# Optimization experiments

Measured on AMD Instinct MI355X. Metric: run time of the kernel, lower is better.

## Reference

```python
import jax, jax.numpy as jnp
import numpy as np

DIM = 1024
HEADS = 16
DIM_HEAD = 64
INNER = HEADS * DIM_HEAD
SCALE = DIM_HEAD ** -0.5
CAUSAL = True


def setup_inputs() -> dict:
    key = jax.random.key(0)
    k1, k2, k3, k4 = jax.random.split(key, 4)
    b, n = 4, 2048
    x = jax.random.normal(k1, (b, n, DIM), dtype=jnp.float32)
    mask = jnp.ones((b, n), dtype=bool)
    w_qkv = jax.random.normal(k2, (DIM, 3 * INNER), dtype=jnp.float32) * (DIM ** -0.5)
    w_out = jax.random.normal(k3, (INNER, DIM), dtype=jnp.float32) * (INNER ** -0.5)
    ln_g = jnp.ones((DIM,), dtype=jnp.float32)
    return {"x": x, "mask": mask, "w_qkv": w_qkv, "w_out": w_out, "ln_g": ln_g}


def clip_layernorm(x, g):
    eps = 1e-5 if x.dtype == jnp.float32 else 1e-3
    mean = jnp.mean(x, axis=-1, keepdims=True)
    var = jnp.var(x, axis=-1, keepdims=True)  # unbiased=False
    return (x - mean) * jax.lax.rsqrt(var + eps) * g


def reference(x, mask, w_qkv, w_out, ln_g):
    b, n, _ = x.shape
    qkv = x @ w_qkv  # [b, n, 3*inner]
    q, k, v = jnp.split(qkv, 3, axis=-1)
    split_heads = lambda t: t.reshape(b, n, HEADS, DIM_HEAD).transpose(0, 2, 1, 3)
    q, k, v = split_heads(q), split_heads(k), split_heads(v)
    q = q * SCALE
    sim = jnp.einsum('bhid,bhjd->bhij', q, k)
    mask_value = -jnp.finfo(sim.dtype).max
    sim = jnp.where(mask[:, None, None, :], sim, mask_value)
    if CAUSAL:
        causal_mask = jnp.triu(jnp.ones((n, n), dtype=bool), k=1)
        sim = jnp.where(causal_mask, mask_value, sim)
    attn = jax.nn.softmax(sim.astype(jnp.float32), axis=-1).astype(sim.dtype)
    out = jnp.einsum('bhij,bhjd->bhid', attn, v)
    out = out.transpose(0, 2, 1, 3).reshape(b, n, INNER)
    out = out @ w_out
    return clip_layernorm(out, ln_g)
```

## Files before the change

kernel.cpp:

```cpp
#include <hip/hip_runtime.h>


typedef unsigned short u16;
typedef __attribute__((ext_vector_type(8))) short bf16x8;
typedef __attribute__((ext_vector_type(4))) float f32x4;
typedef __attribute__((ext_vector_type(4))) unsigned short u16x4;
typedef __attribute__((ext_vector_type(2))) unsigned u32x2;

#define B_SZ  4
#define NSEQ  2048
#define DIMM  1024
#define NQKV  3072
#define MROWS 8192

#define AS_GLOBAL __attribute__((address_space(1)))
#define AS_LDS    __attribute__((address_space(3)))

__device__ __forceinline__ void async_copy16(void* lds, const void* g) {
  __builtin_amdgcn_global_load_lds((const AS_GLOBAL void*)g, (AS_LDS void*)lds, 16, 0, 0);
}

__device__ __forceinline__ u16 f32_to_bf16(float f) {
  unsigned u = __float_as_uint(f);
  u += 0x7FFFu + ((u >> 16) & 1u);
  return (u16)(u >> 16);
}

__device__ __forceinline__ unsigned cvt_pk_bf16(float a, float b) {
  unsigned r;
  asm("v_cvt_pk_bf16_f32 %0, %1, %2" : "=v"(r) : "v"(a), "v"(b));
  return r;
}


__global__ __launch_bounds__(256) void cvt_bf16_k(const float* __restrict__ in,
                                                  u16* __restrict__ out, int n4) {
  int i = blockIdx.x * 256 + threadIdx.x;
  if (i >= n4) return;
  f32x4 v = ((const f32x4*)in)[i];
  u16x4 o;
  #pragma unroll
  for (int c = 0; c < 4; ++c) o[c] = f32_to_bf16(v[c]);
  ((u16x4*)out)[i] = o;
}

__global__ __launch_bounds__(256) void tconv_k(const float* __restrict__ in,
                                               u16* __restrict__ out, int K, int N) {
  __shared__ float tile[64][65];
  int n0 = blockIdx.x * 64, k0 = blockIdx.y * 64;
  int t = threadIdx.x, tr = t >> 6, tc = t & 63;
  #pragma unroll
  for (int i = 0; i < 16; ++i)
    tile[tr + i * 4][tc] = in[(size_t)(k0 + tr + i * 4) * N + n0 + tc];
  __syncthreads();
  #pragma unroll
  for (int i = 0; i < 16; ++i)
    out[(size_t)(n0 + tr + i * 4) * K + k0 + tc] = f32_to_bf16(tile[tc][tr + i * 4]);
}


__device__ __forceinline__ void gemm_tile(const u16* __restrict__ A, const u16* __restrict__ Bt,
                                          int K, size_t arow0, size_t brow0,
                                          u16* lA, u16* lB, int t, f32x4 acc[4][4]) {
  const int w = t >> 6, l = t & 63;
  const int wr = (w >> 1) * 64, wc = (w & 1) * 64;
  const int l4 = l >> 4, l15 = l & 15;
  for (int kt = 0; kt < K; kt += 32) {
    __syncthreads();
    #pragma unroll
    for (int p = 0; p < 2; ++p) {
      int c = p * 256 + t;
      int row = c >> 2, c16 = c & 3;
      async_copy16(&lA[c * 8], &A[(arow0 + row) * (size_t)K + kt + c16 * 8]);
      async_copy16(&lB[c * 8], &Bt[(brow0 + row) * (size_t)K + kt + c16 * 8]);
    }
    __syncthreads();
    bf16x8 af[4], bfr[4];
    #pragma unroll
    for (int i = 0; i < 4; ++i) af[i] = *(const bf16x8*)&lA[(wr + i * 16 + l15) * 32 + l4 * 8];
    #pragma unroll
    for (int j = 0; j < 4; ++j) bfr[j] = *(const bf16x8*)&lB[(wc + j * 16 + l15) * 32 + l4 * 8];
    #pragma unroll
    for (int i = 0; i < 4; ++i)
      #pragma unroll
      for (int j = 0; j < 4; ++j)
        acc[i][j] = __builtin_amdgcn_mfma_f32_16x16x32_bf16(af[i], bfr[j], acc[i][j], 0, 0, 0);
  }
}

__global__ __launch_bounds__(256) void gemm_qkv_k(const u16* __restrict__ A, const u16* __restrict__ Bt,
                                                  u16* __restrict__ qb, u16* __restrict__ kb,
                                                  u16* __restrict__ vtb) {
  __shared__ u16 lA[4096], lB[4096];
  f32x4 acc[4][4];
  #pragma unroll
  for (int i = 0; i < 4; ++i)
    #pragma unroll
    for (int j = 0; j < 4; ++j) acc[i][j] = (f32x4){0.f, 0.f, 0.f, 0.f};
  const int t = threadIdx.x;
  gemm_tile(A, Bt, DIMM, (size_t)blockIdx.y * 128, (size_t)blockIdx.x * 128, lA, lB, t, acc);
  const int w = t >> 6, l = t & 63;
  const int wr = (w >> 1) * 64, wc = (w & 1) * 64;
  const int l4 = l >> 4, l15 = l & 15;
  const float QSCALE = 0.125f * 1.44269504089f;
  #pragma unroll
  for (int i = 0; i < 4; ++i)
    #pragma unroll
    for (int j = 0; j < 4; ++j)
      #pragma unroll
      for (int r = 0; r < 4; ++r) {
        int row = blockIdx.y * 128 + wr + i * 16 + l4 * 4 + r;
        int col = blockIdx.x * 128 + wc + j * 16 + l15;
        float v = acc[i][j][r];
        int bb = row >> 11, nr = row & 2047;
        int part = col >> 10, rem = col & 1023;
        int h = rem >> 6, d = rem & 63;
        int bh = bb * 16 + h;
        if (part == 0)      qb[((size_t)bh * NSEQ + nr) * 64 + d] = f32_to_bf16(v * QSCALE);
        else if (part == 1) kb[((size_t)bh * NSEQ + nr) * 64 + d] = f32_to_bf16(v);
        else                vtb[((size_t)bh * 64 + d) * NSEQ + nr] = f32_to_bf16(v);
      }
}

__global__ __launch_bounds__(256) void gemm_out_k(const u16* __restrict__ A, const u16* __restrict__ Bt,
                                                  float* __restrict__ C) {
  __shared__ u16 lA[4096], lB[4096];
  f32x4 acc[4][4];
  #pragma unroll
  for (int i = 0; i < 4; ++i)
    #pragma unroll
    for (int j = 0; j < 4; ++j) acc[i][j] = (f32x4){0.f, 0.f, 0.f, 0.f};
  const int t = threadIdx.x;
  gemm_tile(A, Bt, DIMM, (size_t)blockIdx.y * 128, (size_t)blockIdx.x * 128, lA, lB, t, acc);
  const int w = t >> 6, l = t & 63;
  const int wr = (w >> 1) * 64, wc = (w & 1) * 64;
  const int l4 = l >> 4, l15 = l & 15;
  #pragma unroll
  for (int i = 0; i < 4; ++i)
    #pragma unroll
    for (int j = 0; j < 4; ++j)
      #pragma unroll
      for (int r = 0; r < 4; ++r) {
        int row = blockIdx.y * 128 + wr + i * 16 + l4 * 4 + r;
        int col = blockIdx.x * 128 + wc + j * 16 + l15;
        C[(size_t)row * DIMM + col] = acc[i][j][r];
      }
}


__global__ __launch_bounds__(512, 4) void attn_k(const u16* __restrict__ qb, const u16* __restrict__ kb,
                                                 const u16* __restrict__ vtb, u16* __restrict__ ao) {
  __shared__ u16 lK[2][64 * 64];
  __shared__ u16 lV[2][64 * 64];
  __shared__ u16 lP[8][16 * 64];
  const int bh = blockIdx.y;
  const int t = threadIdx.x, w = t >> 6, l = t & 63;
  const int l4 = l >> 4, l15 = l & 15;
  const int b = bh >> 4, h = bh & 15;
  u16* lPw = lP[w];

  const int srow = t >> 3;
  const int ssc = (t & 7) ^ (srow & 7);

  #pragma unroll 1
  for (int phase = 0; phase < 2; ++phase) {
    const int qt = phase == 0 ? (int)blockIdx.x : 15 - (int)blockIdx.x;
    const int q0w = qt * 128 + w * 16;

    bf16x8 qf0 = *(const bf16x8*)&qb[((size_t)bh * NSEQ + q0w + l15) * 64 + l4 * 8];
    bf16x8 qf1 = *(const bf16x8*)&qb[((size_t)bh * NSEQ + q0w + l15) * 64 + 32 + l4 * 8];

    float m_r = -1e30f, l_r = 0.f;
    f32x4 o[4];
    #pragma unroll
    for (int d = 0; d < 4; ++d) o[d] = (f32x4){0.f, 0.f, 0.f, 0.f};

    const int njt = 2 * qt + 2;

    {
      async_copy16(&lK[0][t * 8], &kb[((size_t)bh * NSEQ + srow) * 64 + ssc * 8]);
      async_copy16(&lV[0][t * 8], &vtb[((size_t)bh * 64 + srow) * NSEQ + ssc * 8]);
    }
    int buf = 0;

    for (int jt = 0; jt < njt; ++jt) {
      __syncthreads();
      if (jt + 1 < njt) {
        int bsel = buf ^ 1, jn = jt + 1;
        async_copy16(&lK[bsel][t * 8], &kb[((size_t)bh * NSEQ + jn * 64 + srow) * 64 + ssc * 8]);
        async_copy16(&lV[bsel][t * 8], &vtb[((size_t)bh * 64 + srow) * NSEQ + (size_t)jn * 64 + ssc * 8]);
      }
      const int jt64 = jt * 64;
      if (jt64 > q0w + 15) { buf ^= 1; continue; }
      const u16* Kb = lK[buf];
      const u16* Vb = lV[buf];

      bf16x8 kf[4][2];
      #pragma unroll
      for (int nf = 0; nf < 4; ++nf)
        #pragma unroll
        for (int kk = 0; kk < 2; ++kk)
          kf[nf][kk] = *(const bf16x8*)&Kb[(nf * 16 + l15) * 64 + ((kk * 4 + l4) ^ (l15 & 7)) * 8];

      f32x4 z[4];
      __builtin_amdgcn_s_setprio(1);
      #pragma unroll
      for (int nf = 0; nf < 4; ++nf) {
        f32x4 zz = (f32x4){0.f, 0.f, 0.f, 0.f};
        zz = __builtin_amdgcn_mfma_f32_16x16x32_bf16(kf[nf][0], qf0, zz, 0, 0, 0);
        zz = __builtin_amdgcn_mfma_f32_16x16x32_bf16(kf[nf][1], qf1, zz, 0, 0, 0);
        z[nf] = zz;
      }
      __builtin_amdgcn_s_setprio(0);

      bf16x8 bv[4][2];
      #pragma unroll
      for (int dd = 0; dd < 4; ++dd)
        #pragma unroll
        for (int kk = 0; kk < 2; ++kk)
          bv[dd][kk] = *(const bf16x8*)&Vb[(dd * 16 + l15) * 64 + ((kk * 4 + l4) ^ (l15 & 7)) * 8];

      if (jt64 + 63 > q0w) {
        #pragma unroll
        for (int nf = 0; nf < 4; ++nf)
          #pragma unroll
          for (int r = 0; r < 4; ++r)
            if (jt64 + nf * 16 + l4 * 4 + r > q0w + l15) z[nf][r] = -1e30f;
      }

      float mt = fmaxf(fmaxf(z[0][0], z[0][1]), fmaxf(z[0][2], z[0][3]));
      #pragma unroll
      for (int nf = 1; nf < 4; ++nf)
        mt = fmaxf(mt, fmaxf(fmaxf(z[nf][0], z[nf][1]), fmaxf(z[nf][2], z[nf][3])));
      mt = fmaxf(mt, __shfl_xor(mt, 16));
      mt = fmaxf(mt, __shfl_xor(mt, 32));

      if (!__all(mt <= m_r + 8.f)) {
        float nm = fmaxf(m_r, mt);
        float sc = __builtin_amdgcn_exp2f(m_r - nm);
        m_r = nm;
        l_r *= sc;
        float scr[4];
        #pragma unroll
        for (int r = 0; r < 4; ++r) scr[r] = __shfl(sc, l4 * 4 + r);
        #pragma unroll
        for (int d = 0; d < 4; ++d)
          #pragma unroll
          for (int r = 0; r < 4; ++r) o[d][r] *= scr[r];
      }

      float rs = 0.f;
      unsigned pk[4][2];
      #pragma unroll
      for (int nf = 0; nf < 4; ++nf)
        #pragma unroll
        for (int hh = 0; hh < 2; ++hh) {
          float p0 = __builtin_amdgcn_exp2f(z[nf][2 * hh]     - m_r);
          float p1 = __builtin_amdgcn_exp2f(z[nf][2 * hh + 1] - m_r);
          rs += p0 + p1;
          pk[nf][hh] = cvt_pk_bf16(p0, p1);
        }
      rs += __shfl_xor(rs, 16);
      rs += __shfl_xor(rs, 32);
      l_r += rs;

      #pragma unroll
      for (int nf = 0; nf < 4; ++nf) {
        int u = (2 * nf + (l4 >> 1)) ^ (l15 & 7);
        *(u32x2*)&lPw[l15 * 64 + u * 8 + (l4 & 1) * 4] = (u32x2){pk[nf][0], pk[nf][1]};
      }
      __builtin_amdgcn_sched_barrier(0);
      int u0 = l4 ^ (l15 & 7), u1 = (4 + l4) ^ (l15 & 7);
      bf16x8 af0 = *(const bf16x8*)&lPw[l15 * 64 + u0 * 8];
      bf16x8 af1 = *(const bf16x8*)&lPw[l15 * 64 + u1 * 8];

      __builtin_amdgcn_s_setprio(1);
      #pragma unroll
      for (int d = 0; d < 4; ++d) {
        o[d] = __builtin_amdgcn_mfma_f32_16x16x32_bf16(af0, bv[d][0], o[d], 0, 0, 0);
        o[d] = __builtin_amdgcn_mfma_f32_16x16x32_bf16(af1, bv[d][1], o[d], 0, 0, 0);
      }
      __builtin_amdgcn_s_setprio(0);
      buf ^= 1;
    }

    float lv[4];
    #pragma unroll
    for (int r = 0; r < 4; ++r) lv[r] = __shfl(l_r, l4 * 4 + r);
    #pragma unroll
    for (int d = 0; d < 4; ++d)
      #pragma unroll
      for (int r = 0; r < 4; ++r) {
        int nrow = q0w + l4 * 4 + r;
        float vv = o[d][r] / lv[r];
        ao[((size_t)(b * NSEQ + nrow)) * 1024 + h * 64 + d * 16 + l15] = f32_to_bf16(vv);
      }
  }
}

__global__ __launch_bounds__(256) void ln_k(float* __restrict__ io, const float* __restrict__ g) {
  const int row = blockIdx.x, t = threadIdx.x;
  const int w = t >> 6, l = t & 63;
  f32x4 v = ((const f32x4*)(io + (size_t)row * DIMM))[t];
  float s = v[0] + v[1] + v[2] + v[3];
  float q = v[0] * v[0] + v[1] * v[1] + v[2] * v[2] + v[3] * v[3];
  #pragma unroll
  for (int off = 1; off < 64; off <<= 1) { s += __shfl_xor(s, off); q += __shfl_xor(q, off); }
  __shared__ float ss[8];
  if (l == 0) { ss[w] = s; ss[4 + w] = q; }
  __syncthreads();
  s = ss[0] + ss[1] + ss[2] + ss[3];
  q = ss[4] + ss[5] + ss[6] + ss[7];
  float mean = s * (1.f / DIMM);
  float var = q * (1.f / DIMM) - mean * mean;
  float rstd = rsqrtf(var + 1e-5f);
  f32x4 gv = ((const f32x4*)g)[t];
  f32x4 y;
  #pragma unroll
  for (int c = 0; c < 4; ++c) y[c] = (v[c] - mean) * rstd * gv[c];
  ((f32x4*)(io + (size_t)row * DIMM))[t] = y;
}

extern "C" void kernel_launch(void* const* d_in, const int* in_sizes, int n_in,
                              void* d_out, int out_size, void* d_ws, size_t ws_size,
                              hipStream_t stream) {
  const float* x     = (const float*)d_in[0];
  const float* w_qkv = (const float*)d_in[2];
  const float* w_out = (const float*)d_in[3];
  const float* ln_g  = (const float*)d_in[4];
  float* out = (float*)d_out;

  char* ws = (char*)d_ws;
  const size_t MB = 1u << 20;
  u16* x_bf   = (u16*)(ws);
  u16* wqkv_t = (u16*)(ws + 16 * MB);
  u16* wout_t = (u16*)(ws + 22 * MB);
  u16* qb     = (u16*)(ws + 24 * MB);
  u16* kb     = (u16*)(ws + 40 * MB);
  u16* vtb    = (u16*)(ws + 56 * MB);
  u16* attn_o = x_bf;

  cvt_bf16_k<<<8192, 256, 0, stream>>>(x, x_bf, (MROWS * DIMM) / 4);
  tconv_k<<<dim3(NQKV / 64, DIMM / 64), 256, 0, stream>>>(w_qkv, wqkv_t, DIMM, NQKV);
  tconv_k<<<dim3(DIMM / 64, DIMM / 64), 256, 0, stream>>>(w_out, wout_t, DIMM, DIMM);
  gemm_qkv_k<<<dim3(NQKV / 128, MROWS / 128), 256, 0, stream>>>(x_bf, wqkv_t, qb, kb, vtb);
  attn_k<<<dim3(8, B_SZ * 16), 512, 0, stream>>>(qb, kb, vtb, attn_o);
  gemm_out_k<<<dim3(DIMM / 128, MROWS / 128), 256, 0, stream>>>(attn_o, wout_t, out);
  ln_k<<<MROWS, 256, 0, stream>>>(out, ln_g);
}
```

Measured before the change: 210.8 us.

## Triple-buffer GEMM LDS tiles with async prefetch and XOR swizzle

The shared GEMM tile loop now uses a three-stage LDS ring buffer. Global-to-LDS async copies for step s+2 are issued while MFMAs run on step s, with a single barrier per step gated by vmcnt waits. LDS columns are XOR-swizzled to reduce bank conflicts, and MFMA sections are wrapped in s_setprio. This hides global load latency in both the QKV and output projection GEMMs, at the cost of three times the LDS per block, which may reduce occupancy.

```diff
diff --git a/kernel.cpp b/kernel.cpp
--- a/kernel.cpp
+++ b/kernel.cpp
@@ -65,33 +65,69 @@
   const int w = t >> 6, l = t & 63;
   const int wr = (w >> 1) * 64, wc = (w & 1) * 64;
   const int l4 = l >> 4, l15 = l & 15;
-  for (int kt = 0; kt < K; kt += 32) {
-    __syncthreads();
-    #pragma unroll
-    for (int p = 0; p < 2; ++p) {
-      int c = p * 256 + t;
-      int row = c >> 2, c16 = c & 3;
-      async_copy16(&lA[c * 8], &A[(arow0 + row) * (size_t)K + kt + c16 * 8]);
-      async_copy16(&lB[c * 8], &Bt[(brow0 + row) * (size_t)K + kt + c16 * 8]);
-    }
-    __syncthreads();
+
+  const int r0 = t >> 2;
+  const int r1 = 64 + (t >> 2);
+  const int c3 = t & 3;
+  const int sc0 = c3 ^ ((r0 >> 1) & 3);
+  const int sc1 = c3 ^ ((r1 >> 1) & 3);
+
+  auto stage = [&](int kt, int bufi) {
+    u16* dA = lA + bufi * 4096;
+    u16* dB = lB + bufi * 4096;
+    async_copy16(&dA[(size_t)t * 8],         &A[(arow0 + r0) * (size_t)K + kt + sc0 * 8]);
+    async_copy16(&dA[(size_t)(256 + t) * 8], &A[(arow0 + r1) * (size_t)K + kt + sc1 * 8]);
+    async_copy16(&dB[(size_t)t * 8],         &Bt[(brow0 + r0) * (size_t)K + kt + sc0 * 8]);
+    async_copy16(&dB[(size_t)(256 + t) * 8], &Bt[(brow0 + r1) * (size_t)K + kt + sc1 * 8]);
+  };
+
+  const int cs = l4 ^ ((l15 >> 1) & 3);
+
+  auto step = [&](int bufi) {
+    const u16* bA = lA + bufi * 4096;
+    const u16* bB = lB + bufi * 4096;
     bf16x8 af[4], bfr[4];
     #pragma unroll
-    for (int i = 0; i < 4; ++i) af[i] = *(const bf16x8*)&lA[(wr + i * 16 + l15) * 32 + l4 * 8];
-    #pragma unroll
-    for (int j = 0; j < 4; ++j) bfr[j] = *(const bf16x8*)&lB[(wc + j * 16 + l15) * 32 + l4 * 8];
+    for (int i = 0; i < 4; ++i) af[i] = *(const bf16x8*)&bA[(wr + i * 16 + l15) * 32 + cs * 8];
+    #pragma unroll
+    for (int j = 0; j < 4; ++j) bfr[j] = *(const bf16x8*)&bB[(wc + j * 16 + l15) * 32 + cs * 8];
+    __builtin_amdgcn_s_setprio(1);
     #pragma unroll
     for (int i = 0; i < 4; ++i)
       #pragma unroll
       for (int j = 0; j < 4; ++j)
         acc[i][j] = __builtin_amdgcn_mfma_f32_16x16x32_bf16(af[i], bfr[j], acc[i][j], 0, 0, 0);
+    __builtin_amdgcn_s_setprio(0);
+  };
+
+  const int T = K >> 5;
+  stage(0, 0);
+  stage(32, 1);
+  int bc = 0, bn = 2;
+  for (int s = 0; s < T - 2; ++s) {
+    asm volatile("s_waitcnt vmcnt(4)" ::: "memory");
+    __builtin_amdgcn_s_barrier();
+    __builtin_amdgcn_sched_barrier(0);
+    stage((s + 2) * 32, bn);
+    step(bc);
+    bc = bc == 2 ? 0 : bc + 1;
+    bn = bn == 2 ? 0 : bn + 1;
   }
+  asm volatile("s_waitcnt vmcnt(4)" ::: "memory");
+  __builtin_amdgcn_s_barrier();
+  __builtin_amdgcn_sched_barrier(0);
+  step(bc);
+  bc = bc == 2 ? 0 : bc + 1;
+  asm volatile("s_waitcnt vmcnt(0)" ::: "memory");
+  __builtin_amdgcn_s_barrier();
+  __builtin_amdgcn_sched_barrier(0);
+  step(bc);
 }
 
 __global__ __launch_bounds__(256) void gemm_qkv_k(const u16* __restrict__ A, const u16* __restrict__ Bt,
                                                   u16* __restrict__ qb, u16* __restrict__ kb,
                                                   u16* __restrict__ vtb) {
-  __shared__ u16 lA[4096], lB[4096];
+  __shared__ u16 lA[12288], lB[12288];
   f32x4 acc[4][4];
   #pragma unroll
   for (int i = 0; i < 4; ++i)
@@ -124,7 +160,7 @@
 
 __global__ __launch_bounds__(256) void gemm_out_k(const u16* __restrict__ A, const u16* __restrict__ Bt,
                                                   float* __restrict__ C) {
-  __shared__ u16 lA[4096], lB[4096];
+  __shared__ u16 lA[12288], lB[12288];
   f32x4 acc[4][4];
   #pragma unroll
   for (int i = 0; i < 4; ++i)
```

New measurement: 207.6 us. No clear change (-1.5%).

## Rewrite GEMM mainloop with double-buffered swizzled LDS and larger tiles

Applied to the files above, without the earlier changes.

Replaces the single-buffered 128x128 GEMM tile loop with a templated mainloop. It uses K=64 steps, double-buffered LDS with XOR swizzling, and prefetches the next stage while MFMAs run, with setprio hints. The QKV GEMM moves to 256x256 tiles with 512 threads and the output GEMM to 256x128 tiles, so each block reuses more data. The aim is to hide global-load latency, cut bank conflicts and reduce barrier stalls. In exchange it raises register and LDS pressure and launches fewer blocks, which could leave some CUs idle on the smaller output GEMM.

```diff
diff --git a/kernel.cpp b/kernel.cpp
--- a/kernel.cpp
+++ b/kernel.cpp
@@ -59,59 +59,104 @@
 }
 
 
-__device__ __forceinline__ void gemm_tile(const u16* __restrict__ A, const u16* __restrict__ Bt,
-                                          int K, size_t arow0, size_t brow0,
-                                          u16* lA, u16* lB, int t, f32x4 acc[4][4]) {
-  const int w = t >> 6, l = t & 63;
-  const int wr = (w >> 1) * 64, wc = (w & 1) * 64;
-  const int l4 = l >> 4, l15 = l & 15;
-  for (int kt = 0; kt < K; kt += 32) {
-    __syncthreads();
-    #pragma unroll
-    for (int p = 0; p < 2; ++p) {
-      int c = p * 256 + t;
-      int row = c >> 2, c16 = c & 3;
-      async_copy16(&lA[c * 8], &A[(arow0 + row) * (size_t)K + kt + c16 * 8]);
-      async_copy16(&lB[c * 8], &Bt[(brow0 + row) * (size_t)K + kt + c16 * 8]);
-    }
-    __syncthreads();
-    bf16x8 af[4], bfr[4];
-    #pragma unroll
-    for (int i = 0; i < 4; ++i) af[i] = *(const bf16x8*)&lA[(wr + i * 16 + l15) * 32 + l4 * 8];
-    #pragma unroll
-    for (int j = 0; j < 4; ++j) bfr[j] = *(const bf16x8*)&lB[(wc + j * 16 + l15) * 32 + l4 * 8];
-    #pragma unroll
-    for (int i = 0; i < 4; ++i)
-      #pragma unroll
-      for (int j = 0; j < 4; ++j)
-        acc[i][j] = __builtin_amdgcn_mfma_f32_16x16x32_bf16(af[i], bfr[j], acc[i][j], 0, 0, 0);
+template<int WN>
+__device__ __forceinline__ void gemm_mainloop(const u16* __restrict__ A, const u16* __restrict__ Bt,
+                                              int K, size_t arow0, size_t brow0,
+                                              u16* lA, u16* lB, f32x4 acc[8][4]) {
+  constexpr int NW   = 2 * WN;
+  constexpr int BN   = WN * 64;
+  constexpr int ASZ  = 256 * 64;
+  constexpr int BSZ  = BN * 64;
+  constexpr int AIPW = 32 / NW;
+  constexpr int BIPW = (BN / 8) / NW;
+  const int t = threadIdx.x;
+  const int w = t >> 6, lane = t & 63;
+  const int l4 = lane >> 4, l15 = lane & 15;
+  const int wrow = w / WN, wcol = w % WN;
+  const int lr = lane >> 3, lc = lane & 7;
+
+  auto stage = [&](int kt, int bufi) {
+    u16* dA = lA + bufi * ASZ;
+    u16* dB = lB + bufi * BSZ;
+    #pragma unroll
+    for (int j = 0; j < AIPW; ++j) {
+      int r = w * (256 / NW) + j * 8 + lr;
+      async_copy16(&dA[(size_t)r * 64 + lc * 8],
+                   &A[(arow0 + r) * (size_t)K + kt + (lc ^ lr) * 8]);
+    }
+    #pragma unroll
+    for (int j = 0; j < BIPW; ++j) {
+      int r = w * (BN / NW) + j * 8 + lr;
+      async_copy16(&dB[(size_t)r * 64 + lc * 8],
+                   &Bt[(brow0 + r) * (size_t)K + kt + (lc ^ lr) * 8]);
+    }
+  };
+
+  auto phase = [&](int bufi, int ch, bool do_stage, int kt_next, int bufn, bool gate) {
+    const u16* bA = lA + bufi * ASZ;
+    const u16* bB = lB + bufi * BSZ;
+    bf16x8 af[8], bf[4];
+    #pragma unroll
+    for (int m = 0; m < 8; ++m) {
+      int row = wrow * 128 + m * 16 + l15;
+      af[m] = *(const bf16x8*)&bA[(size_t)row * 64 + ((ch * 4 + l4) ^ (row & 7)) * 8];
+    }
+    #pragma unroll
+    for (int n = 0; n < 4; ++n) {
+      int row = wcol * 64 + n * 16 + l15;
+      bf[n] = *(const bf16x8*)&bB[(size_t)row * 64 + ((ch * 4 + l4) ^ (row & 7)) * 8];
+    }
+    if (do_stage) stage(kt_next, bufn);
+    __builtin_amdgcn_s_barrier();
+    asm volatile("s_waitcnt lgkmcnt(0)" ::: "memory");
+    __builtin_amdgcn_sched_barrier(0);
+    __builtin_amdgcn_s_setprio(1);
+    #pragma unroll
+    for (int m = 0; m < 8; ++m)
+      #pragma unroll
+      for (int n = 0; n < 4; ++n)
+        acc[m][n] = __builtin_amdgcn_mfma_f32_16x16x32_bf16(af[m], bf[n], acc[m][n], 0, 0, 0);
+    __builtin_amdgcn_s_setprio(0);
+    if (gate) asm volatile("s_waitcnt vmcnt(0)" ::: "memory");
+    __builtin_amdgcn_s_barrier();
+  };
+
+  const int T = K >> 6;
+  stage(0, 0);
+  asm volatile("s_waitcnt vmcnt(0)" ::: "memory");
+  __builtin_amdgcn_s_barrier();
+  #pragma unroll 1
+  for (int s = 0; s < T; ++s) {
+    const bool st = (s + 1 < T);
+    phase(s & 1, 0, st, (s + 1) * 64, (s + 1) & 1, false);
+    phase(s & 1, 1, false, 0, 0, st);
   }
 }
 
-__global__ __launch_bounds__(256) void gemm_qkv_k(const u16* __restrict__ A, const u16* __restrict__ Bt,
-                                                  u16* __restrict__ qb, u16* __restrict__ kb,
-                                                  u16* __restrict__ vtb) {
-  __shared__ u16 lA[4096], lB[4096];
-  f32x4 acc[4][4];
-  #pragma unroll
-  for (int i = 0; i < 4; ++i)
-    #pragma unroll
-    for (int j = 0; j < 4; ++j) acc[i][j] = (f32x4){0.f, 0.f, 0.f, 0.f};
-  const int t = threadIdx.x;
-  gemm_tile(A, Bt, DIMM, (size_t)blockIdx.y * 128, (size_t)blockIdx.x * 128, lA, lB, t, acc);
-  const int w = t >> 6, l = t & 63;
-  const int wr = (w >> 1) * 64, wc = (w & 1) * 64;
-  const int l4 = l >> 4, l15 = l & 15;
+__global__ __launch_bounds__(512, 2) void gemm_qkv_k(const u16* __restrict__ A, const u16* __restrict__ Bt,
+                                                     u16* __restrict__ qb, u16* __restrict__ kb,
+                                                     u16* __restrict__ vtb) {
+  __shared__ u16 lA[2 * 256 * 64];
+  __shared__ u16 lB[2 * 256 * 64];
+  f32x4 acc[8][4];
+  #pragma unroll
+  for (int m = 0; m < 8; ++m)
+    #pragma unroll
+    for (int n = 0; n < 4; ++n) acc[m][n] = (f32x4){0.f, 0.f, 0.f, 0.f};
+  gemm_mainloop<4>(A, Bt, DIMM, (size_t)blockIdx.y * 256, (size_t)blockIdx.x * 256, lA, lB, acc);
+  const int t = threadIdx.x, w = t >> 6, lane = t & 63;
+  const int l4 = lane >> 4, l15 = lane & 15;
+  const int wrow = w >> 2, wcol = w & 3;
   const float QSCALE = 0.125f * 1.44269504089f;
   #pragma unroll
-  for (int i = 0; i < 4; ++i)
-    #pragma unroll
-    for (int j = 0; j < 4; ++j)
+  for (int m = 0; m < 8; ++m)
+    #pragma unroll
+    for (int n = 0; n < 4; ++n)
       #pragma unroll
       for (int r = 0; r < 4; ++r) {
-        int row = blockIdx.y * 128 + wr + i * 16 + l4 * 4 + r;
-        int col = blockIdx.x * 128 + wc + j * 16 + l15;
-        float v = acc[i][j][r];
+        int row = blockIdx.y * 256 + wrow * 128 + m * 16 + l4 * 4 + r;
+        int col = blockIdx.x * 256 + wcol * 64 + n * 16 + l15;
+        float v = acc[m][n][r];
         int bb = row >> 11, nr = row & 2047;
         int part = col >> 10, rem = col & 1023;
         int h = rem >> 6, d = rem & 63;
@@ -122,28 +167,28 @@
       }
 }
 
-__global__ __launch_bounds__(256) void gemm_out_k(const u16* __restrict__ A, const u16* __restrict__ Bt,
-                                                  float* __restrict__ C) {
-  __shared__ u16 lA[4096], lB[4096];
-  f32x4 acc[4][4];
-  #pragma unroll
-  for (int i = 0; i < 4; ++i)
-    #pragma unroll
-    for (int j = 0; j < 4; ++j) acc[i][j] = (f32x4){0.f, 0.f, 0.f, 0.f};
-  const int t = threadIdx.x;
-  gemm_tile(A, Bt, DIMM, (size_t)blockIdx.y * 128, (size_t)blockIdx.x * 128, lA, lB, t, acc);
-  const int w = t >> 6, l = t & 63;
-  const int wr = (w >> 1) * 64, wc = (w & 1) * 64;
-  const int l4 = l >> 4, l15 = l & 15;
-  #pragma unroll
-  for (int i = 0; i < 4; ++i)
-    #pragma unroll
-    for (int j = 0; j < 4; ++j)
+__global__ __launch_bounds__(256, 1) void gemm_out_k(const u16* __restrict__ A, const u16* __restrict__ Bt,
+                                                     float* __restrict__ C) {
+  __shared__ u16 lA[2 * 256 * 64];
+  __shared__ u16 lB[2 * 128 * 64];
+  f32x4 acc[8][4];
+  #pragma unroll
+  for (int m = 0; m < 8; ++m)
+    #pragma unroll
+    for (int n = 0; n < 4; ++n) acc[m][n] = (f32x4){0.f, 0.f, 0.f, 0.f};
+  gemm_mainloop<2>(A, Bt, DIMM, (size_t)blockIdx.y * 256, (size_t)blockIdx.x * 128, lA, lB, acc);
+  const int t = threadIdx.x, w = t >> 6, lane = t & 63;
+  const int l4 = lane >> 4, l15 = lane & 15;
+  const int wrow = w >> 1, wcol = w & 1;
+  #pragma unroll
+  for (int m = 0; m < 8; ++m)
+    #pragma unroll
+    for (int n = 0; n < 4; ++n)
       #pragma unroll
       for (int r = 0; r < 4; ++r) {
-        int row = blockIdx.y * 128 + wr + i * 16 + l4 * 4 + r;
-        int col = blockIdx.x * 128 + wc + j * 16 + l15;
-        C[(size_t)row * DIMM + col] = acc[i][j][r];
+        int row = blockIdx.y * 256 + wrow * 128 + m * 16 + l4 * 4 + r;
+        int col = blockIdx.x * 128 + wcol * 64 + n * 16 + l15;
+        C[(size_t)row * DIMM + col] = acc[m][n][r];
       }
 }
 
@@ -343,8 +388,8 @@
   cvt_bf16_k<<<8192, 256, 0, stream>>>(x, x_bf, (MROWS * DIMM) / 4);
   tconv_k<<<dim3(NQKV / 64, DIMM / 64), 256, 0, stream>>>(w_qkv, wqkv_t, DIMM, NQKV);
   tconv_k<<<dim3(DIMM / 64, DIMM / 64), 256, 0, stream>>>(w_out, wout_t, DIMM, DIMM);
-  gemm_qkv_k<<<dim3(NQKV / 128, MROWS / 128), 256, 0, stream>>>(x_bf, wqkv_t, qb, kb, vtb);
+  gemm_qkv_k<<<dim3(NQKV / 256, MROWS / 256), 512, 0, stream>>>(x_bf, wqkv_t, qb, kb, vtb);
   attn_k<<<dim3(8, B_SZ * 16), 512, 0, stream>>>(qb, kb, vtb, attn_o);
-  gemm_out_k<<<dim3(DIMM / 128, MROWS / 128), 256, 0, stream>>>(attn_o, wout_t, out);
+  gemm_out_k<<<dim3(DIMM / 128, MROWS / 256), 256, 0, stream>>>(attn_o, wout_t, out);
   ln_k<<<MROWS, 256, 0, stream>>>(out, ln_g);
 }
```

New measurement: 227.2 us. +7.8%, slower.
